# Kernel optimization log

Measured on AMD Instinct MI355X. Metric: run time of the kernel, lower is better.

Reference implementation:

```python
import jax, jax.numpy as jnp
import numpy as np

VOCAB = 50257
EMB = 512
BATCH = 8
SEQ = 4096


def setup_inputs() -> dict:
    key = jax.random.key(0)
    k1, k2 = jax.random.split(key)
    x = jax.random.randint(k1, (BATCH, SEQ), 0, VOCAB, dtype=jnp.int64 if jax.config.jax_enable_x64 else jnp.int32)
    emb = jax.random.normal(k2, (VOCAB, EMB), dtype=jnp.float32)
    return {"x": x, "emb": emb}


def reference(x, emb):
    # scripted loop is equivalent to zeroing even token ids
    x = jnp.where(x % 2 == 0, 0, x)
    # embedding lookup: gather rows of the table
    return emb[x]
```

## Files before the change

### kernel.cpp

```cpp
#include <hip/hip_runtime.h>


#define EMB 512
#define TPW 8

__global__ __launch_bounds__(256) void embed_gather_kernel(
    const int* __restrict__ x,
    const float* __restrict__ emb,
    float* __restrict__ out,
    int n_tokens)
{
    const int wid  = (blockIdx.x * blockDim.x + threadIdx.x) >> 6;
    const int lane = threadIdx.x & 63;
    const int tbase = wid * TPW;
    if (tbase >= n_tokens) return;

    if (tbase + TPW <= n_tokens) {
        int id = x[tbase + (lane & (TPW - 1))];
        id = (id & 1) ? id : 0;

        float4 v[TPW][2];
        #pragma unroll
        for (int i = 0; i < TPW; ++i) {
            const int row = __shfl(id, i, 64);
            const float4* __restrict__ src =
                (const float4*)(emb + (size_t)row * EMB);
            v[i][0] = src[lane];
            v[i][1] = src[lane + 64];
        }
        #pragma unroll
        for (int i = 0; i < TPW; ++i) {
            float4* __restrict__ dst =
                (float4*)(out + (size_t)(tbase + i) * EMB);
            dst[lane]      = v[i][0];
            dst[lane + 64] = v[i][1];
        }
    } else {
        for (int t = tbase; t < n_tokens; ++t) {
            int id = x[t];
            if ((id & 1) == 0) id = 0;
            const float4* __restrict__ src =
                (const float4*)(emb + (size_t)id * EMB);
            float4* __restrict__ dst = (float4*)(out + (size_t)t * EMB);
            dst[lane]      = src[lane];
            dst[lane + 64] = src[lane + 64];
        }
    }
}

extern "C" void kernel_launch(void* const* d_in, const int* in_sizes, int n_in,
                              void* d_out, int out_size, void* d_ws, size_t ws_size,
                              hipStream_t stream)
{
    const int* x = (const int*)d_in[0];
    const float* emb = (const float*)d_in[1];
    float* out = (float*)d_out;

    const int n_tokens = in_sizes[0];
    const int tokens_per_block = (256 / 64) * TPW;
    const int blocks = (n_tokens + tokens_per_block - 1) / tokens_per_block;

    embed_gather_kernel<<<blocks, 256, 0, stream>>>(x, emb, out, n_tokens);
}
```

Measured before the change: 161.3 us.

## Preload row zero, use nontemporal stores, and halve tokens per wave

Each wave loads embedding row 0 once into registers and reuses it for every zeroed (even) token instead of gathering it again. Output writes become nontemporal stores so the large streaming output does not pollute cache, and tokens per wave drops from 8 to 4 for more waves in flight. Row 0 is likely cache-resident already, so the reuse may save little, and the extra branch plus the preload add some overhead.

Result: no change. 162.6 us (+0.8%).

```diff
diff --git a/kernel.cpp b/kernel.cpp
--- a/kernel.cpp
+++ b/kernel.cpp
@@ -2,7 +2,9 @@
 
 
 #define EMB 512
-#define TPW 8
+#define TPW 4
+
+typedef float vf4 __attribute__((ext_vector_type(4)));
 
 __global__ __launch_bounds__(256) void embed_gather_kernel(
     const int* __restrict__ x,
@@ -15,35 +17,46 @@
     const int tbase = wid * TPW;
     if (tbase >= n_tokens) return;
 
+    const vf4* __restrict__ r0 = (const vf4*)emb;
+    const vf4 z0 = r0[lane];
+    const vf4 z1 = r0[lane + 64];
+
     if (tbase + TPW <= n_tokens) {
         int id = x[tbase + (lane & (TPW - 1))];
         id = (id & 1) ? id : 0;
 
-        float4 v[TPW][2];
+        vf4 v[TPW][2];
         #pragma unroll
         for (int i = 0; i < TPW; ++i) {
             const int row = __shfl(id, i, 64);
-            const float4* __restrict__ src =
-                (const float4*)(emb + (size_t)row * EMB);
-            v[i][0] = src[lane];
-            v[i][1] = src[lane + 64];
+            if (row != 0) {
+                const vf4* __restrict__ src = (const vf4*)(emb + (size_t)row * EMB);
+                v[i][0] = src[lane];
+                v[i][1] = src[lane + 64];
+            } else {
+                v[i][0] = z0;
+                v[i][1] = z1;
+            }
         }
         #pragma unroll
         for (int i = 0; i < TPW; ++i) {
-            float4* __restrict__ dst =
-                (float4*)(out + (size_t)(tbase + i) * EMB);
-            dst[lane]      = v[i][0];
-            dst[lane + 64] = v[i][1];
+            vf4* __restrict__ dst = (vf4*)(out + (size_t)(tbase + i) * EMB);
+            __builtin_nontemporal_store(v[i][0], &dst[lane]);
+            __builtin_nontemporal_store(v[i][1], &dst[lane + 64]);
         }
     } else {
         for (int t = tbase; t < n_tokens; ++t) {
             int id = x[t];
             if ((id & 1) == 0) id = 0;
-            const float4* __restrict__ src =
-                (const float4*)(emb + (size_t)id * EMB);
-            float4* __restrict__ dst = (float4*)(out + (size_t)t * EMB);
-            dst[lane]      = src[lane];
-            dst[lane + 64] = src[lane + 64];
+            vf4* __restrict__ dst = (vf4*)(out + (size_t)t * EMB);
+            if (id != 0) {
+                const vf4* __restrict__ src = (const vf4*)(emb + (size_t)id * EMB);
+                __builtin_nontemporal_store(src[lane],      &dst[lane]);
+                __builtin_nontemporal_store(src[lane + 64], &dst[lane + 64]);
+            } else {
+                __builtin_nontemporal_store(z0, &dst[lane]);
+                __builtin_nontemporal_store(z1, &dst[lane + 64]);
+            }
         }
     }
 }
```
